# Kernel optimization log

Measured on AMD Instinct MI355X. Metric: run time of the kernel, lower is better.

Reference implementation:

```python
import jax, jax.numpy as jnp
import numpy as np

B, S, D, H, O, E, K = 4, 1024, 1024, 2048, 1024, 8, 2
LOAD_BALANCE_WEIGHT = 0.01


def setup_inputs() -> dict:
    key = jax.random.key(0)
    ks = jax.random.split(key, 9)
    scale = 0.02
    return {
        "x": jax.random.normal(ks[0], (B, S, D), jnp.float32),
        "Wg": scale * jax.random.normal(ks[1], (D, E), jnp.float32),
        "bg": jnp.zeros((E,), jnp.float32),
        "W1": scale * jax.random.normal(ks[2], (E, D, H), jnp.float32),
        "b1": jnp.zeros((E, H), jnp.float32),
        "W2": scale * jax.random.normal(ks[3], (E, H, H), jnp.float32),
        "b2": jnp.zeros((E, H), jnp.float32),
        "W3": scale * jax.random.normal(ks[4], (E, H, O), jnp.float32),
        "b3": jnp.zeros((E, O), jnp.float32),
    }


def reference(x, Wg, bg, W1, b1, W2, b2, W3, b3):
    # Eval-mode MoE: no gating noise, dropout is identity.
    b, s, d = x.shape
    e = Wg.shape[1]

    # --- gating: noisy top-k gating (noise off in eval) ---
    raw_gates = x @ Wg + bg                         # [B,S,E]
    topk_logits, topk_idx = jax.lax.top_k(raw_gates, K)  # [B,S,K]
    gates = jax.nn.softmax(topk_logits, axis=-1)    # [B,S,K]

    # Combine weights per expert: scatter top-k gates into [B,S,E].
    onehot = jax.nn.one_hot(topk_idx, e, dtype=x.dtype)      # [B,S,K,E]
    combine = jnp.sum(onehot * gates[..., None], axis=-2)    # [B,S,E]

    # --- expert MLPs (dense grouped GEMM over all tokens) ---
    xt = x.reshape(-1, d)            # [T,D]
    wt = combine.reshape(-1, e)      # [T,E]
    h = jax.nn.relu(jnp.einsum('td,edh->eth', xt, W1) + b1[:, None, :])
    h = jax.nn.relu(jnp.einsum('eth,ehg->etg', h, W2) + b2[:, None, :])
    y = jnp.einsum('eth,eho->eto', h, W3) + b3[:, None, :]   # [E,T,O]
    out = jnp.einsum('te,eto->to', wt, y).reshape(b, s, -1)  # [B,S,O]

    # --- auxiliary losses ---
    gate_probs = jax.nn.softmax(raw_gates, axis=-1)          # [B,S,E]
    avg_gate_probs = gate_probs.mean(axis=(0, 1))            # [E]
    avg_expert_counts = combine.mean(axis=(0, 1))            # [E]
    load_balance_loss = LOAD_BALANCE_WEIGHT * e * jnp.sum(avg_gate_probs * avg_expert_counts)
    gate_entropy = -jnp.sum(avg_gate_probs * jnp.log(avg_gate_probs + 1e-8))

    return out, load_balance_loss, avg_expert_counts, gate_entropy
```

## Files before the change

### kernel.cpp

```cpp
#include <hip/hip_runtime.h>
#include <hip/hip_bf16.h>
#include <math.h>

#define T_TOK 4096
#define D_IN  1024
#define H_DIM 2048
#define O_DIM 1024
#define NE    8
#define ROWCAP 9216
#define RT128  72

typedef __bf16 bf16x8 __attribute__((ext_vector_type(8)));
typedef __bf16 bf16x4 __attribute__((ext_vector_type(4)));
typedef float  f32x4  __attribute__((ext_vector_type(4)));

__device__ __forceinline__ void gl_lds16(const void* g, void* l) {
    __builtin_amdgcn_global_load_lds(
        (const __attribute__((address_space(1))) void*)g,
        (__attribute__((address_space(3))) void*)l, 16, 0, 0);
}

__global__ __launch_bounds__(256) void gating_kernel(
    const float* __restrict__ x, const float* __restrict__ Wg, const float* __restrict__ bg,
    __bf16* __restrict__ xb, float* __restrict__ gates_tk, int* __restrict__ idx_tk,
    int* __restrict__ counts, double* __restrict__ prob_part, double* __restrict__ gsum_part)
{
    __shared__ float WgS[8][1032];
    __shared__ float bgS[NE];
    __shared__ double tok_p[32][NE];
    __shared__ double tok_g[32][2];
    __shared__ int    tok_i[32][2];
    const int tid = threadIdx.x;

    for (int i = tid; i < D_IN * NE; i += 256)
        WgS[i >> 10][i & 1023] = Wg[i];
    if (tid < NE) bgS[tid] = bg[tid];

    {
        const size_t base = (size_t)blockIdx.x * 32 * D_IN;
        for (int i = tid * 4; i < 32 * D_IN; i += 256 * 4) {
            float4 v = *(const float4*)(x + base + i);
            bf16x4 b = {(__bf16)v.x, (__bf16)v.y, (__bf16)v.z, (__bf16)v.w};
            *(bf16x4*)(xb + base + i) = b;
        }
    }
    __syncthreads();

    const int tokL = tid >> 3;
    const int part = tid & 7;
    const int t = blockIdx.x * 32 + tokL;
    const float* xr = x + (size_t)t * D_IN + part * 128;

    double s[NE] = {0, 0, 0, 0, 0, 0, 0, 0};
    for (int j = 0; j < 128; j += 4) {
        float4 xv = *(const float4*)(xr + j);
        const float* w = &WgS[part][j * 8];
        #pragma unroll
        for (int jj = 0; jj < 4; ++jj) {
            double xd = (double)((&xv.x)[jj]);
            #pragma unroll
            for (int e = 0; e < NE; ++e)
                s[e] += xd * (double)w[jj * 8 + e];
        }
    }
    #pragma unroll
    for (int off = 4; off; off >>= 1)
        #pragma unroll
        for (int e = 0; e < NE; ++e)
            s[e] += __shfl_xor(s[e], off);

    if (part == 0) {
        double rg[NE];
        #pragma unroll
        for (int e = 0; e < NE; ++e) rg[e] = s[e] + (double)bgS[e];
        int i0 = 0;
        #pragma unroll
        for (int e = 1; e < NE; ++e) if (rg[e] > rg[i0]) i0 = e;
        int i1 = -1;
        #pragma unroll
        for (int e = 0; e < NE; ++e) {
            if (e == i0) continue;
            if (i1 < 0 || rg[e] > rg[i1]) i1 = e;
        }
        double e1 = exp(rg[i1] - rg[i0]);
        double den = 1.0 + e1;
        gates_tk[t * 2] = (float)(1.0 / den); gates_tk[t * 2 + 1] = (float)(e1 / den);
        idx_tk[t * 2] = i0;   idx_tk[t * 2 + 1] = i1;
        tok_g[tokL][0] = 1.0 / den; tok_g[tokL][1] = e1 / den;
        tok_i[tokL][0] = i0;        tok_i[tokL][1] = i1;
        double mx = rg[0];
        #pragma unroll
        for (int e = 1; e < NE; ++e) mx = fmax(mx, rg[e]);
        double pe[NE], sum = 0.0;
        #pragma unroll
        for (int e = 0; e < NE; ++e) { pe[e] = exp(rg[e] - mx); sum += pe[e]; }
        #pragma unroll
        for (int e = 0; e < NE; ++e) tok_p[tokL][e] = pe[e] / sum;
    }
    __syncthreads();
    if (tid < NE) {
        double p = 0.0, g = 0.0; int c = 0;
        for (int i = 0; i < 32; ++i) {
            p += tok_p[i][tid];
            if (tok_i[i][0] == tid) { g += tok_g[i][0]; ++c; }
            if (tok_i[i][1] == tid) { g += tok_g[i][1]; ++c; }
        }
        prob_part[blockIdx.x * NE + tid] = p;
        gsum_part[blockIdx.x * NE + tid] = g;
        atomicAdd(&counts[tid], c);
    }
}

__global__ __launch_bounds__(256) void transpose_cvt(
    const float* __restrict__ src, __bf16* __restrict__ dst, int K, int N)
{
    const int e = blockIdx.z;
    src += (size_t)e * K * N;
    dst += (size_t)e * N * K;
    const int k0 = blockIdx.y * 64, n0 = blockIdx.x * 64;
    __shared__ float tile[64][65];
    const int tid = threadIdx.x;
    const int r = tid >> 4;
    const int c = (tid & 15) * 4;
    #pragma unroll
    for (int i = 0; i < 4; ++i) {
        float4 v = *(const float4*)(src + (size_t)(k0 + r + i * 16) * N + n0 + c);
        tile[r + i * 16][c + 0] = v.x;
        tile[r + i * 16][c + 1] = v.y;
        tile[r + i * 16][c + 2] = v.z;
        tile[r + i * 16][c + 3] = v.w;
    }
    __syncthreads();
    const int n = tid >> 2;
    const int kc = (tid & 3) * 16;
    bf16x8 v0, v1;
    #pragma unroll
    for (int j = 0; j < 8; ++j) v0[j] = (__bf16)tile[kc + j][n];
    #pragma unroll
    for (int j = 0; j < 8; ++j) v1[j] = (__bf16)tile[kc + 8 + j][n];
    __bf16* dp = dst + (size_t)(n0 + n) * K + k0 + kc;
    *(bf16x8*)dp = v0;
    *(bf16x8*)(dp + 8) = v1;
}

__global__ void build_offsets(const int* __restrict__ counts, int* __restrict__ poffset,
                              int* __restrict__ totalp, int* __restrict__ token_ids)
{
    __shared__ int po[NE + 1];
    __shared__ int cnt[NE];
    const int tid = threadIdx.x;
    if (tid == 0) {
        po[0] = 0;
        for (int e = 0; e < NE; ++e) {
            cnt[e] = counts[e];
            int pc = (cnt[e] + 127) & ~127;
            po[e + 1] = po[e] + pc;
        }
        for (int e = 0; e <= NE; ++e) poffset[e] = po[e];
        totalp[0] = po[NE];
    }
    __syncthreads();
    for (int e = 0; e < NE; ++e) {
        int base = po[e], c = cnt[e], pc = po[e + 1] - po[e];
        for (int i = c + tid; i < pc; i += 64) token_ids[base + i] = 0;
    }
}

__global__ __launch_bounds__(256) void scatter_rows(
    const int* __restrict__ idx_tk, const int* __restrict__ poffset,
    int* __restrict__ cursors, int* __restrict__ token_ids, int* __restrict__ t2r)
{
    int t = blockIdx.x * 256 + threadIdx.x;
    if (t >= T_TOK) return;
    for (int k = 0; k < 2; ++k) {
        int e = idx_tk[t * 2 + k];
        int pos = atomicAdd(&cursors[e], 1);
        int r = poffset[e] + pos;
        token_ids[r] = t;
        t2r[t * 2 + k] = r;
    }
}

template<bool GATHER, bool RELU, bool OUTBF16>
__global__ __launch_bounds__(256) void gemm_expert(
    const __bf16* __restrict__ A, int lda,
    const __bf16* __restrict__ Bt, int Kdim, int N,
    const float* __restrict__ bias,
    void* __restrict__ Out, int ldo,
    const int* __restrict__ token_ids,
    const int* __restrict__ poffset,
    const int* __restrict__ totalp)
{
    __shared__ __bf16 As[128 * 64];
    __shared__ __bf16 Bs[128 * 64];
    const int tid = threadIdx.x;
    const int row0 = blockIdx.y * 128;
    if (row0 >= totalp[0]) return;
    int e = 0;
    while (e < NE - 1 && row0 >= poffset[e + 1]) ++e;
    const int n0 = blockIdx.x * 128;
    const __bf16* Be = Bt + (size_t)e * Kdim * N;
    const float* biase = bias + (size_t)e * N;

    const int srow = tid >> 3;
    const int jperm = (tid & 7) ^ (srow & 7);
    const int scol = jperm * 8;
    int arow_g[4];
    #pragma unroll
    for (int c = 0; c < 4; ++c) {
        int r = row0 + c * 32 + srow;
        arow_g[c] = GATHER ? token_ids[r] : r;
    }
    const __bf16* bbase = Be + (size_t)(n0 + srow) * Kdim + scol;

    const int lane = tid & 63;
    const int quad = lane >> 4;
    const int m16  = lane & 15;
    const int wave = tid >> 6;
    const int wm = wave >> 1, wn = wave & 1;

    f32x4 acc[4][4];
    #pragma unroll
    for (int i = 0; i < 4; ++i)
        #pragma unroll
        for (int j = 0; j < 4; ++j)
            acc[i][j] = (f32x4){0.f, 0.f, 0.f, 0.f};

    const int niter = Kdim >> 6;
    for (int kt = 0; kt < niter; ++kt) {
        const int kofs = kt * 64 + scol;
        #pragma unroll
        for (int c = 0; c < 4; ++c)
            gl_lds16(A + (size_t)arow_g[c] * lda + kofs, (char*)As + c * 4096 + tid * 16);
        #pragma unroll
        for (int c = 0; c < 4; ++c)
            gl_lds16(bbase + (size_t)c * 32 * Kdim + kt * 64, (char*)Bs + c * 4096 + tid * 16);
        __syncthreads();
        #pragma unroll
        for (int ks = 0; ks < 2; ++ks) {
            const int p = ((ks << 2) | quad) ^ (m16 & 7);
            bf16x8 af[4], bfr[4];
            #pragma unroll
            for (int i = 0; i < 4; ++i)
                af[i] = *(const bf16x8*)&As[(wm * 64 + i * 16 + m16) * 64 + p * 8];
            #pragma unroll
            for (int j = 0; j < 4; ++j)
                bfr[j] = *(const bf16x8*)&Bs[(wn * 64 + j * 16 + m16) * 64 + p * 8];
            #pragma unroll
            for (int i = 0; i < 4; ++i)
                #pragma unroll
                for (int j = 0; j < 4; ++j)
                    acc[i][j] = __builtin_amdgcn_mfma_f32_16x16x32_bf16(af[i], bfr[j], acc[i][j], 0, 0, 0);
        }
        __syncthreads();
    }
    #pragma unroll
    for (int i = 0; i < 4; ++i)
        #pragma unroll
        for (int j = 0; j < 4; ++j)
            #pragma unroll
            for (int r = 0; r < 4; ++r) {
                int grow = row0 + wm * 64 + i * 16 + quad * 4 + r;
                int gcol = n0 + wn * 64 + j * 16 + m16;
                float v = acc[i][j][r] + biase[gcol];
                if (RELU) v = v > 0.f ? v : 0.f;
                if (OUTBF16) ((__bf16*)Out)[(size_t)grow * ldo + gcol] = (__bf16)v;
                else         ((float*)Out)[(size_t)grow * ldo + gcol] = v;
            }
}

__global__ __launch_bounds__(256) void combine_out(
    const float* __restrict__ y, const float* __restrict__ gates_tk,
    const int* __restrict__ t2r, float* __restrict__ out)
{
    const int t = blockIdx.x;
    const int o = threadIdx.x * 4;
    const int r0 = t2r[t * 2], r1 = t2r[t * 2 + 1];
    const float g0 = gates_tk[t * 2], g1 = gates_tk[t * 2 + 1];
    float4 a = *(const float4*)&y[(size_t)r0 * O_DIM + o];
    float4 b = *(const float4*)&y[(size_t)r1 * O_DIM + o];
    float4 c;
    c.x = g0 * a.x + g1 * b.x;
    c.y = g0 * a.y + g1 * b.y;
    c.z = g0 * a.z + g1 * b.z;
    c.w = g0 * a.w + g1 * b.w;
    *(float4*)&out[(size_t)t * O_DIM + o] = c;
}

__global__ void finalize_kernel(const double* __restrict__ prob_part,
                                const double* __restrict__ gsum_part,
                                float* __restrict__ out)
{
    __shared__ double ps[NE], gs[NE];
    const int tid = threadIdx.x;
    if (tid < NE) {
        double p = 0.0, g = 0.0;
        for (int b = 0; b < 128; ++b) {
            p += prob_part[b * NE + tid];
            g += gsum_part[b * NE + tid];
        }
        ps[tid] = p / (double)T_TOK;
        gs[tid] = g / (double)T_TOK;
        out[(size_t)T_TOK * O_DIM + 1 + tid] = (float)(g / (double)T_TOK);
    }
    __syncthreads();
    if (tid == 0) {
        double lb = 0.0, ent = 0.0;
        for (int e = 0; e < NE; ++e) {
            lb += ps[e] * gs[e];
            ent -= ps[e] * log(ps[e] + 1e-8);
        }
        out[(size_t)T_TOK * O_DIM] = (float)(0.01 * 8.0 * lb);
        out[(size_t)T_TOK * O_DIM + 9] = (float)ent;
    }
}

extern "C" void kernel_launch(void* const* d_in, const int* in_sizes, int n_in,
                              void* d_out, int out_size, void* d_ws, size_t ws_size,
                              hipStream_t stream)
{
    const float* x  = (const float*)d_in[0];
    const float* Wg = (const float*)d_in[1];
    const float* bg = (const float*)d_in[2];
    const float* W1 = (const float*)d_in[3];
    const float* b1 = (const float*)d_in[4];
    const float* W2 = (const float*)d_in[5];
    const float* b2 = (const float*)d_in[6];
    const float* W3 = (const float*)d_in[7];
    const float* b3 = (const float*)d_in[8];
    float* out = (float*)d_out;
    char* ws = (char*)d_ws;

    size_t off = 0;
    __bf16* xb  = (__bf16*)(ws + off); off += (size_t)T_TOK * D_IN * 2;
    __bf16* h1  = (__bf16*)(ws + off);
    float*  y   = (float*) (ws + off); off += (size_t)ROWCAP * H_DIM * 2;
    __bf16* h2  = (__bf16*)(ws + off); off += (size_t)ROWCAP * H_DIM * 2;
    __bf16* W1t = (__bf16*)(ws + off); off += (size_t)NE * H_DIM * D_IN * 2;
    __bf16* W2t = (__bf16*)(ws + off); off += (size_t)NE * H_DIM * H_DIM * 2;
    __bf16* W3t = (__bf16*)(ws + off); off += (size_t)NE * O_DIM * H_DIM * 2;
    float* gates_tk = (float*)(ws + off); off += T_TOK * 2 * 4;
    int* idx_tk     = (int*)(ws + off);   off += T_TOK * 2 * 4;
    int* t2r        = (int*)(ws + off);   off += T_TOK * 2 * 4;
    int* token_ids  = (int*)(ws + off);   off += ROWCAP * 4;
    double* prob_part = (double*)(ws + off); off += 128 * NE * 8;
    double* gsum_part = (double*)(ws + off); off += 128 * NE * 8;
    char* small     = ws + off;
    int* counts     = (int*)(small + 0);
    int* cursors    = (int*)(small + 32);
    int* poffset    = (int*)(small + 64);
    int* totalp     = (int*)(small + 112);

    hipMemsetAsync(small, 0, 256, stream);
    gating_kernel<<<128, 256, 0, stream>>>(x, Wg, bg, xb, gates_tk, idx_tk,
                                           counts, prob_part, gsum_part);
    transpose_cvt<<<dim3(H_DIM / 64, D_IN / 64, NE), 256, 0, stream>>>(W1, W1t, D_IN, H_DIM);
    transpose_cvt<<<dim3(H_DIM / 64, H_DIM / 64, NE), 256, 0, stream>>>(W2, W2t, H_DIM, H_DIM);
    transpose_cvt<<<dim3(O_DIM / 64, H_DIM / 64, NE), 256, 0, stream>>>(W3, W3t, H_DIM, O_DIM);
    build_offsets<<<1, 64, 0, stream>>>(counts, poffset, totalp, token_ids);
    scatter_rows<<<16, 256, 0, stream>>>(idx_tk, poffset, cursors, token_ids, t2r);
    gemm_expert<true,  true,  true ><<<dim3(H_DIM / 128, RT128), 256, 0, stream>>>(
        xb, D_IN, W1t, D_IN, H_DIM, b1, (void*)h1, H_DIM, token_ids, poffset, totalp);
    gemm_expert<false, true,  true ><<<dim3(H_DIM / 128, RT128), 256, 0, stream>>>(
        h1, H_DIM, W2t, H_DIM, H_DIM, b2, (void*)h2, H_DIM, token_ids, poffset, totalp);
    gemm_expert<false, false, false><<<dim3(O_DIM / 128, RT128), 256, 0, stream>>>(
        h2, H_DIM, W3t, H_DIM, O_DIM, b3, (void*)y, O_DIM, token_ids, poffset, totalp);
    combine_out<<<T_TOK, 256, 0, stream>>>(y, gates_tk, t2r, out);
    finalize_kernel<<<1, 64, 0, stream>>>(prob_part, gsum_part, out);
}
```

Measured before the change: 644.7 us.

## Fuse weight transpose and bf16 conversion into expert GEMM B-tile loads

Removes the three transpose_cvt pre-pass kernels and their bf16 weight workspace. Each GEMM now loads fp32 weights straight from their original layout into registers, converts them to bf16, and writes them transposed and swizzled into LDS. The next tile is register-prefetched after the barrier so it overlaps the MFMA work. In exchange, every row-tile block re-reads fp32 weights, doubling weight bytes per GEMM, and does conversion and scattered LDS stores inside the main loop.

```diff
diff --git a/kernel.cpp b/kernel.cpp
--- a/kernel.cpp
+++ b/kernel.cpp
@@ -14,6 +14,8 @@
 typedef __bf16 bf16x4 __attribute__((ext_vector_type(4)));
 typedef float  f32x4  __attribute__((ext_vector_type(4)));
 
+#define ELT(f, j) ((j) == 0 ? (f).x : (j) == 1 ? (f).y : (j) == 2 ? (f).z : (f).w)
+
 __device__ __forceinline__ void gl_lds16(const void* g, void* l) {
     __builtin_amdgcn_global_load_lds(
         (const __attribute__((address_space(1))) void*)g,
@@ -57,7 +59,7 @@
         const float* w = &WgS[part][j * 8];
         #pragma unroll
         for (int jj = 0; jj < 4; ++jj) {
-            double xd = (double)((&xv.x)[jj]);
+            double xd = (double)(ELT(xv, jj));
             #pragma unroll
             for (int e = 0; e < NE; ++e)
                 s[e] += xd * (double)w[jj * 8 + e];
@@ -109,38 +111,6 @@
         gsum_part[blockIdx.x * NE + tid] = g;
         atomicAdd(&counts[tid], c);
     }
-}
-
-__global__ __launch_bounds__(256) void transpose_cvt(
-    const float* __restrict__ src, __bf16* __restrict__ dst, int K, int N)
-{
-    const int e = blockIdx.z;
-    src += (size_t)e * K * N;
-    dst += (size_t)e * N * K;
-    const int k0 = blockIdx.y * 64, n0 = blockIdx.x * 64;
-    __shared__ float tile[64][65];
-    const int tid = threadIdx.x;
-    const int r = tid >> 4;
-    const int c = (tid & 15) * 4;
-    #pragma unroll
-    for (int i = 0; i < 4; ++i) {
-        float4 v = *(const float4*)(src + (size_t)(k0 + r + i * 16) * N + n0 + c);
-        tile[r + i * 16][c + 0] = v.x;
-        tile[r + i * 16][c + 1] = v.y;
-        tile[r + i * 16][c + 2] = v.z;
-        tile[r + i * 16][c + 3] = v.w;
-    }
-    __syncthreads();
-    const int n = tid >> 2;
-    const int kc = (tid & 3) * 16;
-    bf16x8 v0, v1;
-    #pragma unroll
-    for (int j = 0; j < 8; ++j) v0[j] = (__bf16)tile[kc + j][n];
-    #pragma unroll
-    for (int j = 0; j < 8; ++j) v1[j] = (__bf16)tile[kc + 8 + j][n];
-    __bf16* dp = dst + (size_t)(n0 + n) * K + k0 + kc;
-    *(bf16x8*)dp = v0;
-    *(bf16x8*)(dp + 8) = v1;
 }
 
 __global__ void build_offsets(const int* __restrict__ counts, int* __restrict__ poffset,
@@ -184,7 +154,7 @@
 template<bool GATHER, bool RELU, bool OUTBF16>
 __global__ __launch_bounds__(256) void gemm_expert(
     const __bf16* __restrict__ A, int lda,
-    const __bf16* __restrict__ Bt, int Kdim, int N,
+    const float* __restrict__ Bw, int Kdim, int N,
     const float* __restrict__ bias,
     void* __restrict__ Out, int ldo,
     const int* __restrict__ token_ids,
@@ -199,7 +169,7 @@
     int e = 0;
     while (e < NE - 1 && row0 >= poffset[e + 1]) ++e;
     const int n0 = blockIdx.x * 128;
-    const __bf16* Be = Bt + (size_t)e * Kdim * N;
+    const float* Be = Bw + (size_t)e * Kdim * N;
     const float* biase = bias + (size_t)e * N;
 
     const int srow = tid >> 3;
@@ -211,7 +181,10 @@
         int r = row0 + c * 32 + srow;
         arow_g[c] = GATHER ? token_ids[r] : r;
     }
-    const __bf16* bbase = Be + (size_t)(n0 + srow) * Kdim + scol;
+
+    const int rg = tid >> 5;
+    const int cB = tid & 31;
+    const float* bsrc0 = Be + (size_t)rg * 8 * N + n0 + cB * 4;
 
     const int lane = tid & 63;
     const int quad = lane >> 4;
@@ -227,15 +200,32 @@
             acc[i][j] = (f32x4){0.f, 0.f, 0.f, 0.f};
 
     const int niter = Kdim >> 6;
+
+    float4 r[8];
+    #pragma unroll
+    for (int i = 0; i < 8; ++i)
+        r[i] = *(const float4*)(bsrc0 + (size_t)i * N);
+
     for (int kt = 0; kt < niter; ++kt) {
         const int kofs = kt * 64 + scol;
         #pragma unroll
         for (int c = 0; c < 4; ++c)
             gl_lds16(A + (size_t)arow_g[c] * lda + kofs, (char*)As + c * 4096 + tid * 16);
         #pragma unroll
-        for (int c = 0; c < 4; ++c)
-            gl_lds16(bbase + (size_t)c * 32 * Kdim + kt * 64, (char*)Bs + c * 4096 + tid * 16);
+        for (int j = 0; j < 4; ++j) {
+            const int n = cB * 4 + j;
+            bf16x8 v;
+            #pragma unroll
+            for (int i = 0; i < 8; ++i) v[i] = (__bf16)(ELT(r[i], j));
+            *(bf16x8*)&Bs[n * 64 + ((rg ^ (n & 7)) << 3)] = v;
+        }
         __syncthreads();
+        if (kt + 1 < niter) {
+            const float* bsrc = bsrc0 + (size_t)(kt + 1) * 64 * N;
+            #pragma unroll
+            for (int i = 0; i < 8; ++i)
+                r[i] = *(const float4*)(bsrc + (size_t)i * N);
+        }
         #pragma unroll
         for (int ks = 0; ks < 2; ++ks) {
             const int p = ((ks << 2) | quad) ^ (m16 & 7);
@@ -259,10 +249,10 @@
         #pragma unroll
         for (int j = 0; j < 4; ++j)
             #pragma unroll
-            for (int r = 0; r < 4; ++r) {
-                int grow = row0 + wm * 64 + i * 16 + quad * 4 + r;
+            for (int rr = 0; rr < 4; ++rr) {
+                int grow = row0 + wm * 64 + i * 16 + quad * 4 + rr;
                 int gcol = n0 + wn * 64 + j * 16 + m16;
-                float v = acc[i][j][r] + biase[gcol];
+                float v = acc[i][j][rr] + biase[gcol];
                 if (RELU) v = v > 0.f ? v : 0.f;
                 if (OUTBF16) ((__bf16*)Out)[(size_t)grow * ldo + gcol] = (__bf16)v;
                 else         ((float*)Out)[(size_t)grow * ldo + gcol] = v;
@@ -336,9 +326,6 @@
     __bf16* h1  = (__bf16*)(ws + off);
     float*  y   = (float*) (ws + off); off += (size_t)ROWCAP * H_DIM * 2;
     __bf16* h2  = (__bf16*)(ws + off); off += (size_t)ROWCAP * H_DIM * 2;
-    __bf16* W1t = (__bf16*)(ws + off); off += (size_t)NE * H_DIM * D_IN * 2;
-    __bf16* W2t = (__bf16*)(ws + off); off += (size_t)NE * H_DIM * H_DIM * 2;
-    __bf16* W3t = (__bf16*)(ws + off); off += (size_t)NE * O_DIM * H_DIM * 2;
     float* gates_tk = (float*)(ws + off); off += T_TOK * 2 * 4;
     int* idx_tk     = (int*)(ws + off);   off += T_TOK * 2 * 4;
     int* t2r        = (int*)(ws + off);   off += T_TOK * 2 * 4;
@@ -354,17 +341,14 @@
     hipMemsetAsync(small, 0, 256, stream);
     gating_kernel<<<128, 256, 0, stream>>>(x, Wg, bg, xb, gates_tk, idx_tk,
                                            counts, prob_part, gsum_part);
-    transpose_cvt<<<dim3(H_DIM / 64, D_IN / 64, NE), 256, 0, stream>>>(W1, W1t, D_IN, H_DIM);
-    transpose_cvt<<<dim3(H_DIM / 64, H_DIM / 64, NE), 256, 0, stream>>>(W2, W2t, H_DIM, H_DIM);
-    transpose_cvt<<<dim3(O_DIM / 64, H_DIM / 64, NE), 256, 0, stream>>>(W3, W3t, H_DIM, O_DIM);
     build_offsets<<<1, 64, 0, stream>>>(counts, poffset, totalp, token_ids);
     scatter_rows<<<16, 256, 0, stream>>>(idx_tk, poffset, cursors, token_ids, t2r);
     gemm_expert<true,  true,  true ><<<dim3(H_DIM / 128, RT128), 256, 0, stream>>>(
-        xb, D_IN, W1t, D_IN, H_DIM, b1, (void*)h1, H_DIM, token_ids, poffset, totalp);
+        xb, D_IN, W1, D_IN, H_DIM, b1, (void*)h1, H_DIM, token_ids, poffset, totalp);
     gemm_expert<false, true,  true ><<<dim3(H_DIM / 128, RT128), 256, 0, stream>>>(
-        h1, H_DIM, W2t, H_DIM, H_DIM, b2, (void*)h2, H_DIM, token_ids, poffset, totalp);
+        h1, H_DIM, W2, H_DIM, H_DIM, b2, (void*)h2, H_DIM, token_ids, poffset, totalp);
     gemm_expert<false, false, false><<<dim3(O_DIM / 128, RT128), 256, 0, stream>>>(
-        h2, H_DIM, W3t, H_DIM, O_DIM, b3, (void*)y, O_DIM, token_ids, poffset, totalp);
+        h2, H_DIM, W3, H_DIM, O_DIM, b3, (void*)y, O_DIM, token_ids, poffset, totalp);
     combine_out<<<T_TOK, 256, 0, stream>>>(y, gates_tk, t2r, out);
     finalize_kernel<<<1, 64, 0, stream>>>(prob_part, gsum_part, out);
 }
```

New measurement: 631.3 us. 2.1% less time.
